# Performance work log

Hardware: AMD Instinct MI355X
Metric: run time of the kernel (lower is better)

The kernel has to match this reference:

```python
import jax, jax.numpy as jnp
import numpy as np

N_NODES = 50000
N_EDGES = 800000
HEADS = 4
IN_CH = 128
HID_CH = 32   # per-head, conv1
OUT_CH = 32   # per-head, conv2
N_GRAPHS = 64
NEG_SLOPE = 0.2
BN_EPS = 1e-5


def gat_conv(x, src, dst, n_nodes, W, att_src, att_dst, bias):
    """PyG-style GATConv (concat heads). x:[N,Fin], W:[Fin,H*C], att_*:[H,C], bias:[H*C]."""
    H, C = att_src.shape
    h = (x @ W).reshape(n_nodes, H, C)                      # [N,H,C]
    a_src = jnp.einsum('nhc,hc->nh', h, att_src)            # [N,H]
    a_dst = jnp.einsum('nhc,hc->nh', h, att_dst)            # [N,H]
    e = jax.nn.leaky_relu(a_src[src] + a_dst[dst], NEG_SLOPE)  # [E,H]
    # segment softmax over incoming edges of each destination node
    e_max = jax.ops.segment_max(e, dst, num_segments=n_nodes)  # [N,H]
    alpha = jnp.exp(e - e_max[dst])                         # [E,H]
    denom = jax.ops.segment_sum(alpha, dst, num_segments=n_nodes)  # [N,H]
    alpha = alpha / denom[dst]
    msg = alpha[:, :, None] * h[src]                        # [E,H,C]
    out = jax.ops.segment_sum(msg, dst, num_segments=n_nodes)  # [N,H,C]
    return out.reshape(n_nodes, H * C) + bias


def setup_inputs() -> dict:
    key = jax.random.key(0)
    ks = jax.random.split(key, 12)
    d1 = HID_CH * HEADS  # 128
    d2 = OUT_CH * HEADS  # 128
    s_in = 1.0 / np.sqrt(IN_CH)
    s_h = 1.0 / np.sqrt(d1)
    return {
        'x': jax.random.normal(ks[0], (N_NODES, IN_CH), jnp.float32),
        'edge_index': jax.random.randint(ks[1], (2, N_EDGES), 0, N_NODES, jnp.int32),
        'batch': jnp.sort(jax.random.randint(ks[2], (N_NODES,), 0, N_GRAPHS, jnp.int32)),
        'W1': jax.random.normal(ks[3], (IN_CH, d1), jnp.float32) * s_in,
        'att_src1': jax.random.normal(ks[4], (HEADS, HID_CH), jnp.float32) * s_h,
        'att_dst1': jax.random.normal(ks[5], (HEADS, HID_CH), jnp.float32) * s_h,
        'bias1': jnp.zeros((d1,), jnp.float32),
        'gamma1': jnp.ones((d1,), jnp.float32),
        'beta1': jnp.zeros((d1,), jnp.float32),
        'W2': jax.random.normal(ks[6], (d1, d2), jnp.float32) * s_h,
        'att_src2': jax.random.normal(ks[7], (HEADS, OUT_CH), jnp.float32) * s_h,
        'att_dst2': jax.random.normal(ks[8], (HEADS, OUT_CH), jnp.float32) * s_h,
        'bias2': jnp.zeros((d2,), jnp.float32),
    }


def reference(x, edge_index, batch, W1, att_src1, att_dst1, bias1,
              gamma1, beta1, W2, att_src2, att_dst2, bias2):
    n = x.shape[0]
    loops = jnp.arange(n, dtype=edge_index.dtype)
    src = jnp.concatenate([edge_index[0], loops])  # add self-loops (PyG default)
    dst = jnp.concatenate([edge_index[1], loops])

    h = gat_conv(x, src, dst, n, W1, att_src1, att_dst1, bias1)
    # BatchNorm1d (batch statistics, biased variance), then ELU; dropout is inference no-op
    mu = h.mean(axis=0)
    var = h.var(axis=0)
    h = (h - mu) * jax.lax.rsqrt(var + BN_EPS) * gamma1 + beta1
    h = jax.nn.elu(h)

    h2 = gat_conv(h, src, dst, n, W2, att_src2, att_dst2, bias2)  # [N, OUT_CH*HEADS]

    # global mean pool over graphs
    ones = jnp.ones((n,), h2.dtype)
    counts = jax.ops.segment_sum(ones, batch, num_segments=N_GRAPHS)
    pooled = jax.ops.segment_sum(h2, batch, num_segments=N_GRAPHS)
    graph_rep = pooled / jnp.maximum(counts, 1.0)[:, None]
    return (h2, graph_rep)
```

## Files before the change

kernel.cpp:

```cpp
#include <hip/hip_runtime.h>

#define NN 50000
#define NE 800000
#define ET 850000
#define NG 64
#define D  128
#define NB 196
#define CAP 5120
#define CHUNK 8192

typedef unsigned short u16;
typedef unsigned int   u32;
typedef short bf16x8 __attribute__((ext_vector_type(8)));
typedef float f32x4  __attribute__((ext_vector_type(4)));

__device__ __forceinline__ u16 f2b(float f){
  u32 u = __float_as_uint(f);
  u32 r = (u + 0x7fffu + ((u >> 16) & 1u)) >> 16;
  return (u16)r;
}
__device__ __forceinline__ u32 pack2(float a, float b){
  return (u32)f2b(a) | ((u32)f2b(b) << 16);
}
__device__ __forceinline__ float lo16f(u32 u){ return __uint_as_float(u << 16); }
__device__ __forceinline__ float hi16f(u32 u){ return __uint_as_float(u & 0xffff0000u); }

__global__ void k_init(int* gCur, float* bsum, float* bsq, float* pooled){
  int i = blockIdx.x*256 + threadIdx.x;
  if (i < 256) gCur[i] = 0;
  if (i < 128){ bsum[i] = 0.f; bsq[i] = 0.f; }
  if (i < NG*D) pooled[i] = 0.f;
}

__global__ __launch_bounds__(256) void k_bucket(const int* __restrict__ srcE, const int* __restrict__ dstE,
                                                int* __restrict__ gCur, int* __restrict__ temp){
  __shared__ int hist[256], hbase[256], hpos[256], gbase[256];
  __shared__ int sorted[CHUNK];
  int tid = threadIdx.x;
  int e0 = blockIdx.x * CHUNK;
  int e1 = e0 + CHUNK; if (e1 > NE) e1 = NE;
  int cnt = e1 - e0;
  hist[tid] = 0;
  __syncthreads();
  for (int i = e0 + tid; i < e1; i += 256)
    atomicAdd(&hist[(u32)dstE[i] >> 8], 1);
  __syncthreads();
  int v = hist[tid];
  hbase[tid] = v;
  __syncthreads();
  for (int off = 1; off < 256; off <<= 1){
    int t = (tid >= off) ? hbase[tid-off] : 0;
    __syncthreads();
    hbase[tid] += t;
    __syncthreads();
  }
  int excl = hbase[tid] - v;
  __syncthreads();
  hbase[tid] = excl;
  hpos[tid]  = excl;
  __syncthreads();
  for (int i = e0 + tid; i < e1; i += 256){
    int d = dstE[i], sr = srcE[i];
    int idx = atomicAdd(&hpos[(u32)d >> 8], 1);
    sorted[idx] = (d << 16) | sr;
  }
  __syncthreads();
  if (tid < NB && hist[tid] > 0)
    gbase[tid] = atomicAdd(&gCur[tid], hist[tid]);
  __syncthreads();
  for (int i = tid; i < cnt; i += 256){
    int vv = sorted[i];
    int b = (u32)vv >> 24;
    int pos = gbase[b] + (i - hbase[b]);
    if (pos < CAP) temp[b*CAP + pos] = vv;
  }
}

__global__ void k_bstart(const int* __restrict__ gCur, int* __restrict__ bstart, int* __restrict__ offs){
  __shared__ int s[256];
  int tid = threadIdx.x;
  int nodes = (tid < NB) ? ((tid == NB-1) ? (NN - (NB-1)*256) : 256) : 0;
  int v = (tid < NB) ? gCur[tid] + nodes : 0;
  s[tid] = v;
  __syncthreads();
  for (int off = 1; off < 256; off <<= 1){
    int t = (tid >= off) ? s[tid-off] : 0;
    __syncthreads();
    s[tid] += t;
    __syncthreads();
  }
  if (tid < NB) bstart[tid] = s[tid] - v;
  if (tid == 0) offs[NN] = ET;
}

__global__ __launch_bounds__(256) void k_place(const int* __restrict__ temp, const int* __restrict__ gCur,
                                               const int* __restrict__ bstart, int* __restrict__ offs,
                                               int* __restrict__ srcs){
  __shared__ int cnt256[256], pfx[256], pos[256];
  int b = blockIdx.x, tid = threadIdx.x;
  int n0 = b << 8;
  int nNodes = NN - n0; if (nNodes > 256) nNodes = 256;
  int count = gCur[b];
  const int* tb = temp + b*CAP;
  cnt256[tid] = 0;
  __syncthreads();
  for (int i = tid; i < count; i += 256)
    atomicAdd(&cnt256[((u32)tb[i] >> 16) & 255], 1);
  __syncthreads();
  int own = cnt256[tid] + (tid < nNodes ? 1 : 0);
  pfx[tid] = own;
  __syncthreads();
  for (int off = 1; off < 256; off <<= 1){
    int t = (tid >= off) ? pfx[tid-off] : 0;
    __syncthreads();
    pfx[tid] += t;
    __syncthreads();
  }
  int excl = pfx[tid] - own;
  __syncthreads();
  pos[tid] = excl + 1;
  __syncthreads();
  int base = bstart[b];
  if (tid < nNodes){
    offs[n0 + tid] = base + excl;
    srcs[base + excl] = n0 + tid;
  }
  for (int i = tid; i < count; i += 256){
    int vv = tb[i];
    int d = ((u32)vv >> 16) & 255;
    int k = atomicAdd(&pos[d], 1);
    srcs[base + k] = vv & 0xFFFF;
  }
}

template<int FUSE_BN>
__global__ __launch_bounds__(512) void k_gemm(const float* __restrict__ X, const float* __restrict__ W,
                                              u16* __restrict__ Ybf,
                                              const float* __restrict__ att_s, const float* __restrict__ att_d,
                                              float* __restrict__ asrc, float* __restrict__ adst,
                                              const float* __restrict__ bsc, const float* __restrict__ bsh,
                                              int nrows){
  __shared__ u16 Xs[64*132];
  __shared__ u16 WT[128*132];
  int tid = threadIdx.x;
  int row0 = blockIdx.x * 64;
  {
    int r = tid >> 3, k4 = tid & 7;
    int gr = row0 + r;
    #pragma unroll
    for (int t = 0; t < 4; t++){
      int kidx = k4 + t*8;
      float4 v = (gr < nrows) ? ((const float4*)(X + (size_t)gr*D))[kidx]
                              : make_float4(0.f,0.f,0.f,0.f);
      if (FUSE_BN){
        float4 sc = ((const float4*)bsc)[kidx];
        float4 sh = ((const float4*)bsh)[kidx];
        v.x = fmaf(v.x, sc.x, sh.x); v.y = fmaf(v.y, sc.y, sh.y);
        v.z = fmaf(v.z, sc.z, sh.z); v.w = fmaf(v.w, sc.w, sh.w);
        v.x = v.x > 0.f ? v.x : expm1f(v.x);
        v.y = v.y > 0.f ? v.y : expm1f(v.y);
        v.z = v.z > 0.f ? v.z : expm1f(v.z);
        v.w = v.w > 0.f ? v.w : expm1f(v.w);
      }
      *(uint2*)&Xs[r*132 + kidx*4] = make_uint2(pack2(v.x, v.y), pack2(v.z, v.w));
    }
  }
  {
    int c = tid & 127, kp = tid >> 7;
    #pragma unroll
    for (int t = 0; t < 16; t++){
      int kk = kp + t*4;
      float w0 = W[(size_t)(2*kk)*D + c];
      float w1 = W[(size_t)(2*kk+1)*D + c];
      *(u32*)&WT[c*132 + 2*kk] = pack2(w0, w1);
    }
  }
  __syncthreads();
  int w = tid >> 6, l = tid & 63;
  int l15 = l & 15, lq = l >> 4;
  int cw = w*16;
  bf16x8 bfr[4];
  #pragma unroll
  for (int ks = 0; ks < 4; ks++)
    bfr[ks] = *(const bf16x8*)&WT[(cw + l15)*132 + ks*32 + lq*8];
  f32x4 acc[4];
  #pragma unroll
  for (int m = 0; m < 4; m++) acc[m] = (f32x4){0.f,0.f,0.f,0.f};
  #pragma unroll
  for (int m = 0; m < 4; m++){
    #pragma unroll
    for (int ks = 0; ks < 4; ks++){
      bf16x8 af = *(const bf16x8*)&Xs[(m*16 + l15)*132 + ks*32 + lq*8];
      acc[m] = __builtin_amdgcn_mfma_f32_16x16x32_bf16(af, bfr[ks], acc[m], 0, 0, 0);
    }
  }
  __syncthreads();
  float* sDotS = (float*)Xs;
  float* sDotD = sDotS + 512;
  {
    float as_c = att_s[cw + l15];
    float ad_c = att_d[cw + l15];
    #pragma unroll
    for (int m = 0; m < 4; m++){
      #pragma unroll
      for (int i = 0; i < 4; i++){
        float ps = acc[m][i] * as_c;
        float pd = acc[m][i] * ad_c;
        #pragma unroll
        for (int msk = 1; msk <= 8; msk <<= 1){
          ps += __shfl_xor(ps, msk);
          pd += __shfl_xor(pd, msk);
        }
        if (l15 == 0){
          int r = m*16 + lq*4 + i;
          sDotS[w*64 + r] = ps;
          sDotD[w*64 + r] = pd;
        }
      }
    }
  }
  #pragma unroll
  for (int m = 0; m < 4; m++){
    #pragma unroll
    for (int i = 0; i < 4; i++){
      float v = acc[m][i];
      float nb = __shfl_xor(v, 1);
      if (!(l & 1)){
        int gr = row0 + m*16 + lq*4 + i;
        if (gr < nrows)
          *(u32*)&Ybf[(size_t)gr*D + cw + l15] = pack2(v, nb);
      }
    }
  }
  __syncthreads();
  if (tid < 256){
    int r = tid >> 2, h = tid & 3;
    int gr = row0 + r;
    if (gr < nrows){
      asrc[gr*4 + h] = sDotS[(2*h)*64 + r] + sDotS[(2*h+1)*64 + r];
      adst[gr*4 + h] = sDotD[(2*h)*64 + r] + sDotD[(2*h+1)*64 + r];
    }
  }
}

__global__ __launch_bounds__(256) void k_edge(
                       const u16* __restrict__ hb, const float* __restrict__ asrc,
                       const float* __restrict__ adst, const int* __restrict__ offs,
                       const int* __restrict__ srcs, const float* __restrict__ bias,
                       float* __restrict__ out){
  __shared__ uint2 sPk[4][4][16];
  int w = threadIdx.x >> 6;
  int lane = threadIdx.x & 63;
  int n = blockIdx.x*4 + w;
  int off0 = offs[n];
  int deg  = offs[n+1] - off0;
  int hd = lane >> 4, j16 = lane & 15;
  float adh = adst[n*4 + hd];
  int half = lane >> 5, q = lane & 31;
  int hg = q >> 3;
  int qb = q*8;
  float denp = 0.f;
  float acc0=0.f, acc1=0.f, acc2=0.f, acc3=0.f;
  const char* hbase = (const char*)hb;
  const int* sp = srcs + off0;
  for (int base = 0; base < deg; base += 16){
    int lim = deg - base; if (lim > 16) lim = 16;
    int sj; float al;
    if (j16 < lim){
      sj = sp[base + j16];
      float e = asrc[sj*4 + hd] + adh;
      e = e > 0.f ? e : 0.2f*e;
      al = __expf(e);
    } else { sj = 0; al = 0.f; }
    denp += al;
    sPk[w][hd][j16] = make_uint2((u32)sj << 8, __float_as_uint(al));
    if (lim == 16){
      uint2 p0 = sPk[w][hg][half],      p1 = sPk[w][hg][2+half];
      uint2 p2 = sPk[w][hg][4+half],    p3 = sPk[w][hg][6+half];
      uint2 p4 = sPk[w][hg][8+half],    p5 = sPk[w][hg][10+half];
      uint2 p6 = sPk[w][hg][12+half],   p7 = sPk[w][hg][14+half];
      uint2 v0 = *(const uint2*)(hbase + p0.x + qb);
      uint2 v1 = *(const uint2*)(hbase + p1.x + qb);
      uint2 v2 = *(const uint2*)(hbase + p2.x + qb);
      uint2 v3 = *(const uint2*)(hbase + p3.x + qb);
      uint2 v4 = *(const uint2*)(hbase + p4.x + qb);
      uint2 v5 = *(const uint2*)(hbase + p5.x + qb);
      uint2 v6 = *(const uint2*)(hbase + p6.x + qb);
      uint2 v7 = *(const uint2*)(hbase + p7.x + qb);
      float a0 = __uint_as_float(p0.y), a1 = __uint_as_float(p1.y);
      float a2 = __uint_as_float(p2.y), a3 = __uint_as_float(p3.y);
      float a4 = __uint_as_float(p4.y), a5 = __uint_as_float(p5.y);
      float a6 = __uint_as_float(p6.y), a7 = __uint_as_float(p7.y);
      acc0 = fmaf(a0, lo16f(v0.x), acc0); acc1 = fmaf(a0, hi16f(v0.x), acc1);
      acc2 = fmaf(a0, lo16f(v0.y), acc2); acc3 = fmaf(a0, hi16f(v0.y), acc3);
      acc0 = fmaf(a1, lo16f(v1.x), acc0); acc1 = fmaf(a1, hi16f(v1.x), acc1);
      acc2 = fmaf(a1, lo16f(v1.y), acc2); acc3 = fmaf(a1, hi16f(v1.y), acc3);
      acc0 = fmaf(a2, lo16f(v2.x), acc0); acc1 = fmaf(a2, hi16f(v2.x), acc1);
      acc2 = fmaf(a2, lo16f(v2.y), acc2); acc3 = fmaf(a2, hi16f(v2.y), acc3);
      acc0 = fmaf(a3, lo16f(v3.x), acc0); acc1 = fmaf(a3, hi16f(v3.x), acc1);
      acc2 = fmaf(a3, lo16f(v3.y), acc2); acc3 = fmaf(a3, hi16f(v3.y), acc3);
      acc0 = fmaf(a4, lo16f(v4.x), acc0); acc1 = fmaf(a4, hi16f(v4.x), acc1);
      acc2 = fmaf(a4, lo16f(v4.y), acc2); acc3 = fmaf(a4, hi16f(v4.y), acc3);
      acc0 = fmaf(a5, lo16f(v5.x), acc0); acc1 = fmaf(a5, hi16f(v5.x), acc1);
      acc2 = fmaf(a5, lo16f(v5.y), acc2); acc3 = fmaf(a5, hi16f(v5.y), acc3);
      acc0 = fmaf(a6, lo16f(v6.x), acc0); acc1 = fmaf(a6, hi16f(v6.x), acc1);
      acc2 = fmaf(a6, lo16f(v6.y), acc2); acc3 = fmaf(a6, hi16f(v6.y), acc3);
      acc0 = fmaf(a7, lo16f(v7.x), acc0); acc1 = fmaf(a7, hi16f(v7.x), acc1);
      acc2 = fmaf(a7, lo16f(v7.y), acc2); acc3 = fmaf(a7, hi16f(v7.y), acc3);
    } else {
      for (int j = 0; j < lim; j += 8){
        uint2 pA = sPk[w][hg][j+half],   pB = sPk[w][hg][j+2+half];
        uint2 pC = sPk[w][hg][j+4+half], pD = sPk[w][hg][j+6+half];
        uint2 vA = *(const uint2*)(hbase + pA.x + qb);
        uint2 vB = *(const uint2*)(hbase + pB.x + qb);
        uint2 vC = *(const uint2*)(hbase + pC.x + qb);
        uint2 vD = *(const uint2*)(hbase + pD.x + qb);
        float aA = __uint_as_float(pA.y), aB = __uint_as_float(pB.y);
        float aC = __uint_as_float(pC.y), aD = __uint_as_float(pD.y);
        acc0 = fmaf(aA, lo16f(vA.x), acc0); acc1 = fmaf(aA, hi16f(vA.x), acc1);
        acc2 = fmaf(aA, lo16f(vA.y), acc2); acc3 = fmaf(aA, hi16f(vA.y), acc3);
        acc0 = fmaf(aB, lo16f(vB.x), acc0); acc1 = fmaf(aB, hi16f(vB.x), acc1);
        acc2 = fmaf(aB, lo16f(vB.y), acc2); acc3 = fmaf(aB, hi16f(vB.y), acc3);
        acc0 = fmaf(aC, lo16f(vC.x), acc0); acc1 = fmaf(aC, hi16f(vC.x), acc1);
        acc2 = fmaf(aC, lo16f(vC.y), acc2); acc3 = fmaf(aC, hi16f(vC.y), acc3);
        acc0 = fmaf(aD, lo16f(vD.x), acc0); acc1 = fmaf(aD, hi16f(vD.x), acc1);
        acc2 = fmaf(aD, lo16f(vD.y), acc2); acc3 = fmaf(aD, hi16f(vD.y), acc3);
      }
    }
  }
  denp += __shfl_xor(denp, 1);
  denp += __shfl_xor(denp, 2);
  denp += __shfl_xor(denp, 4);
  denp += __shfl_xor(denp, 8);
  acc0 += __shfl_xor(acc0, 32);
  acc1 += __shfl_xor(acc1, 32);
  acc2 += __shfl_xor(acc2, 32);
  acc3 += __shfl_xor(acc3, 32);
  float inv = 1.f / __shfl(denp, hg*16);
  if (half == 0){
    int cb = q*4;
    float4 o;
    o.x = acc0*inv + bias[cb];
    o.y = acc1*inv + bias[cb+1];
    o.z = acc2*inv + bias[cb+2];
    o.w = acc3*inv + bias[cb+3];
    ((float4*)(out + (size_t)n*D))[q] = o;
  }
}

__global__ __launch_bounds__(256) void k_bnstat(const float* __restrict__ B,
                                                float* __restrict__ bsum, float* __restrict__ bsq){
  __shared__ float sS[256], sQ[256];
  int tid = threadIdx.x;
  int c = tid & 127;
  int rr = tid >> 7;
  int r0 = blockIdx.x * 64;
  int r1 = r0 + 64; if (r1 > NN) r1 = NN;
  float s = 0.f, qv = 0.f;
  for (int r = r0 + rr; r < r1; r += 2){
    float v = B[(size_t)r*D + c];
    s += v; qv += v*v;
  }
  sS[tid] = s; sQ[tid] = qv;
  __syncthreads();
  if (tid < 128){
    atomicAdd(&bsum[c], sS[tid] + sS[tid+128]);
    atomicAdd(&bsq[c],  sQ[tid] + sQ[tid+128]);
  }
}

__global__ void k_bnfin(const float* __restrict__ bsum, const float* __restrict__ bsq,
                        const float* __restrict__ gamma, const float* __restrict__ beta,
                        float* __restrict__ scale, float* __restrict__ shift){
  int c = threadIdx.x;
  float mu  = bsum[c] * (1.f/NN);
  float var = bsq[c] * (1.f/NN) - mu*mu;
  float sc  = gamma[c] * rsqrtf(var + 1e-5f);
  scale[c] = sc;
  shift[c] = beta[c] - mu*sc;
}

#define POOL_ROWS 50
__global__ void k_poolA(const float* __restrict__ h2, const int* __restrict__ batch,
                        float* __restrict__ pooled){
  int c = threadIdx.x & 127;
  int half = threadIdx.x >> 7;
  int r0 = blockIdx.x * POOL_ROWS;
  int r1 = r0 + POOL_ROWS; if (r1 > NN) r1 = NN;
  float s = 0.f; int g = -1;
  for (int r = r0 + half; r < r1; r += 2){
    int bg = batch[r];
    if (bg != g){
      if (g >= 0) atomicAdd(&pooled[g*D + c], s);
      g = bg; s = 0.f;
    }
    s += h2[(size_t)r*D + c];
  }
  if (g >= 0) atomicAdd(&pooled[g*D + c], s);
}

__global__ void k_poolB(const float* __restrict__ pooled, const int* __restrict__ batch,
                        float* __restrict__ out){
  int g = blockIdx.x;
  int c = threadIdx.x;
  int lo = 0, hi = NN;
  while (lo < hi){ int mid = (lo+hi) >> 1; if (batch[mid] < g) lo = mid+1; else hi = mid; }
  int a = lo, b = NN;
  while (a < b){ int mid = (a+b) >> 1; if (batch[mid] < g+1) a = mid+1; else b = mid; }
  int cntg = a - lo;
  out[g*D + c] = pooled[g*D + c] / (float)(cntg > 1 ? cntg : 1);
}

extern "C" void kernel_launch(void* const* d_in, const int* in_sizes, int n_in,
                              void* d_out, int out_size, void* d_ws, size_t ws_size,
                              hipStream_t stream){
  (void)in_sizes; (void)n_in; (void)out_size; (void)ws_size;
  const float* x   = (const float*)d_in[0];
  const int* ei    = (const int*)d_in[1];
  const int* batch = (const int*)d_in[2];
  const float* W1  = (const float*)d_in[3];
  const float* as1 = (const float*)d_in[4];
  const float* ad1 = (const float*)d_in[5];
  const float* b1  = (const float*)d_in[6];
  const float* g1  = (const float*)d_in[7];
  const float* be1 = (const float*)d_in[8];
  const float* W2  = (const float*)d_in[9];
  const float* as2 = (const float*)d_in[10];
  const float* ad2 = (const float*)d_in[11];
  const float* b2  = (const float*)d_in[12];
  float* outp = (float*)d_out;

  float* B    = (float*)d_ws;
  float* asr  = B + 6400000;
  float* ads  = asr + 200000;
  float* bsum = ads + 200000;
  float* bsq  = bsum + 128;
  float* bsc  = bsq + 128;
  float* bsh  = bsc + 128;
  float* pooled = bsh + 128;
  int* gCur   = (int*)(pooled + NG*D);
  int* bstart = gCur + 256;
  int* offs   = bstart + 256;
  int* srcs   = offs + (NN+1);
  int* temp   = srcs + ET;
  u16* hb     = (u16*)(temp + NB*CAP);

  const int* srcE = ei;
  const int* dstE = ei + NE;

  k_init<<<32, 256, 0, stream>>>(gCur, bsum, bsq, pooled);
  k_gemm<0><<<782, 512, 0, stream>>>(x, W1, hb, as1, ad1, asr, ads, nullptr, nullptr, NN);
  k_bucket<<<(NE + CHUNK - 1)/CHUNK, 256, 0, stream>>>(srcE, dstE, gCur, temp);
  k_bstart<<<1, 256, 0, stream>>>(gCur, bstart, offs);
  k_place<<<NB, 256, 0, stream>>>(temp, gCur, bstart, offs, srcs);
  k_edge<<<NN/4, 256, 0, stream>>>(hb, asr, ads, offs, srcs, b1, B);
  k_bnstat<<<782, 256, 0, stream>>>(B, bsum, bsq);
  k_bnfin<<<1, 128, 0, stream>>>(bsum, bsq, g1, be1, bsc, bsh);
  k_gemm<1><<<782, 512, 0, stream>>>(B, W2, hb, as2, ad2, asr, ads, bsc, bsh, NN);
  k_edge<<<NN/4, 256, 0, stream>>>(hb, asr, ads, offs, srcs, b2, outp);
  k_poolA<<<(NN + POOL_ROWS - 1)/POOL_ROWS, 256, 0, stream>>>(outp, batch, pooled);
  k_poolB<<<NG, 128, 0, stream>>>(pooled, batch, outp + 6400000);
}
```

Baseline: 232.9 us.

## Double GEMM row tile and prefetch next edge chunk indices in edge kernel

The GEMM kernel now handles 128 rows per block instead of 64, halving the grid and amortising the per-block W transpose/load across more rows, at the cost of more LDS and accumulator registers. The edge kernel software-pipelines the neighbour index and asrc gather for the next 16-edge chunk while the current chunk is processed, hiding the dependent load latency. The shared staging array is padded to 17 to reduce LDS bank conflicts. More registers may lower occupancy.

```diff
diff --git a/kernel.cpp b/kernel.cpp
--- a/kernel.cpp
+++ b/kernel.cpp
@@ -140,30 +140,28 @@
                                               float* __restrict__ asrc, float* __restrict__ adst,
                                               const float* __restrict__ bsc, const float* __restrict__ bsh,
                                               int nrows){
-  __shared__ u16 Xs[64*132];
+  __shared__ u16 Xs[128*132];
   __shared__ u16 WT[128*132];
   int tid = threadIdx.x;
-  int row0 = blockIdx.x * 64;
-  {
-    int r = tid >> 3, k4 = tid & 7;
+  int row0 = blockIdx.x * 128;
+  #pragma unroll
+  for (int t = 0; t < 8; t++){
+    int i = tid + t*512;
+    int r = i >> 5, k4 = i & 31;
     int gr = row0 + r;
-    #pragma unroll
-    for (int t = 0; t < 4; t++){
-      int kidx = k4 + t*8;
-      float4 v = (gr < nrows) ? ((const float4*)(X + (size_t)gr*D))[kidx]
-                              : make_float4(0.f,0.f,0.f,0.f);
-      if (FUSE_BN){
-        float4 sc = ((const float4*)bsc)[kidx];
-        float4 sh = ((const float4*)bsh)[kidx];
-        v.x = fmaf(v.x, sc.x, sh.x); v.y = fmaf(v.y, sc.y, sh.y);
-        v.z = fmaf(v.z, sc.z, sh.z); v.w = fmaf(v.w, sc.w, sh.w);
-        v.x = v.x > 0.f ? v.x : expm1f(v.x);
-        v.y = v.y > 0.f ? v.y : expm1f(v.y);
-        v.z = v.z > 0.f ? v.z : expm1f(v.z);
-        v.w = v.w > 0.f ? v.w : expm1f(v.w);
-      }
-      *(uint2*)&Xs[r*132 + kidx*4] = make_uint2(pack2(v.x, v.y), pack2(v.z, v.w));
-    }
+    float4 v = (gr < nrows) ? ((const float4*)(X + (size_t)gr*D))[k4]
+                            : make_float4(0.f,0.f,0.f,0.f);
+    if (FUSE_BN){
+      float4 sc = ((const float4*)bsc)[k4];
+      float4 sh = ((const float4*)bsh)[k4];
+      v.x = fmaf(v.x, sc.x, sh.x); v.y = fmaf(v.y, sc.y, sh.y);
+      v.z = fmaf(v.z, sc.z, sh.z); v.w = fmaf(v.w, sc.w, sh.w);
+      v.x = v.x > 0.f ? v.x : expm1f(v.x);
+      v.y = v.y > 0.f ? v.y : expm1f(v.y);
+      v.z = v.z > 0.f ? v.z : expm1f(v.z);
+      v.w = v.w > 0.f ? v.w : expm1f(v.w);
+    }
+    *(uint2*)&Xs[r*132 + k4*4] = make_uint2(pack2(v.x, v.y), pack2(v.z, v.w));
   }
   {
     int c = tid & 127, kp = tid >> 7;
@@ -183,11 +181,11 @@
   #pragma unroll
   for (int ks = 0; ks < 4; ks++)
     bfr[ks] = *(const bf16x8*)&WT[(cw + l15)*132 + ks*32 + lq*8];
-  f32x4 acc[4];
+  f32x4 acc[8];
   #pragma unroll
-  for (int m = 0; m < 4; m++) acc[m] = (f32x4){0.f,0.f,0.f,0.f};
+  for (int m = 0; m < 8; m++) acc[m] = (f32x4){0.f,0.f,0.f,0.f};
   #pragma unroll
-  for (int m = 0; m < 4; m++){
+  for (int m = 0; m < 8; m++){
     #pragma unroll
     for (int ks = 0; ks < 4; ks++){
       bf16x8 af = *(const bf16x8*)&Xs[(m*16 + l15)*132 + ks*32 + lq*8];
@@ -196,12 +194,12 @@
   }
   __syncthreads();
   float* sDotS = (float*)Xs;
-  float* sDotD = sDotS + 512;
+  float* sDotD = sDotS + 1024;
   {
     float as_c = att_s[cw + l15];
     float ad_c = att_d[cw + l15];
     #pragma unroll
-    for (int m = 0; m < 4; m++){
+    for (int m = 0; m < 8; m++){
       #pragma unroll
       for (int i = 0; i < 4; i++){
         float ps = acc[m][i] * as_c;
@@ -213,14 +211,14 @@
         }
         if (l15 == 0){
           int r = m*16 + lq*4 + i;
-          sDotS[w*64 + r] = ps;
-          sDotD[w*64 + r] = pd;
+          sDotS[w*128 + r] = ps;
+          sDotD[w*128 + r] = pd;
         }
       }
     }
   }
   #pragma unroll
-  for (int m = 0; m < 4; m++){
+  for (int m = 0; m < 8; m++){
     #pragma unroll
     for (int i = 0; i < 4; i++){
       float v = acc[m][i];
@@ -233,12 +231,12 @@
     }
   }
   __syncthreads();
-  if (tid < 256){
+  {
     int r = tid >> 2, h = tid & 3;
     int gr = row0 + r;
     if (gr < nrows){
-      asrc[gr*4 + h] = sDotS[(2*h)*64 + r] + sDotS[(2*h+1)*64 + r];
-      adst[gr*4 + h] = sDotD[(2*h)*64 + r] + sDotD[(2*h+1)*64 + r];
+      asrc[gr*4 + h] = sDotS[(2*h)*128 + r] + sDotS[(2*h+1)*128 + r];
+      adst[gr*4 + h] = sDotD[(2*h)*128 + r] + sDotD[(2*h+1)*128 + r];
     }
   }
 }
@@ -248,7 +246,7 @@
                        const float* __restrict__ adst, const int* __restrict__ offs,
                        const int* __restrict__ srcs, const float* __restrict__ bias,
                        float* __restrict__ out){
-  __shared__ uint2 sPk[4][4][16];
+  __shared__ uint2 sPk[4][4][17];
   int w = threadIdx.x >> 6;
   int lane = threadIdx.x & 63;
   int n = blockIdx.x*4 + w;
@@ -263,17 +261,26 @@
   float acc0=0.f, acc1=0.f, acc2=0.f, acc3=0.f;
   const char* hbase = (const char*)hb;
   const int* sp = srcs + off0;
+  int sj = (j16 < deg) ? sp[j16] : 0;
+  float av = asrc[sj*4 + hd];
   for (int base = 0; base < deg; base += 16){
     int lim = deg - base; if (lim > 16) lim = 16;
-    int sj; float al;
+    int nbase = base + 16;
+    bool hasn = (nbase < deg);
+    int sjn = 0;
+    if (hasn){
+      int idx = nbase + j16;
+      sjn = (idx < deg) ? sp[idx] : 0;
+    }
+    float al;
     if (j16 < lim){
-      sj = sp[base + j16];
-      float e = asrc[sj*4 + hd] + adh;
+      float e = av + adh;
       e = e > 0.f ? e : 0.2f*e;
       al = __expf(e);
-    } else { sj = 0; al = 0.f; }
+    } else al = 0.f;
     denp += al;
     sPk[w][hd][j16] = make_uint2((u32)sj << 8, __float_as_uint(al));
+    float avn = hasn ? asrc[sjn*4 + hd] : 0.f;
     if (lim == 16){
       uint2 p0 = sPk[w][hg][half],      p1 = sPk[w][hg][2+half];
       uint2 p2 = sPk[w][hg][4+half],    p3 = sPk[w][hg][6+half];
@@ -327,6 +334,7 @@
         acc2 = fmaf(aD, lo16f(vD.y), acc2); acc3 = fmaf(aD, hi16f(vD.y), acc3);
       }
     }
+    sj = sjn; av = avn;
   }
   denp += __shfl_xor(denp, 1);
   denp += __shfl_xor(denp, 2);
@@ -449,14 +457,14 @@
   const int* dstE = ei + NE;
 
   k_init<<<32, 256, 0, stream>>>(gCur, bsum, bsq, pooled);
-  k_gemm<0><<<782, 512, 0, stream>>>(x, W1, hb, as1, ad1, asr, ads, nullptr, nullptr, NN);
+  k_gemm<0><<<391, 512, 0, stream>>>(x, W1, hb, as1, ad1, asr, ads, nullptr, nullptr, NN);
   k_bucket<<<(NE + CHUNK - 1)/CHUNK, 256, 0, stream>>>(srcE, dstE, gCur, temp);
   k_bstart<<<1, 256, 0, stream>>>(gCur, bstart, offs);
   k_place<<<NB, 256, 0, stream>>>(temp, gCur, bstart, offs, srcs);
   k_edge<<<NN/4, 256, 0, stream>>>(hb, asr, ads, offs, srcs, b1, B);
   k_bnstat<<<782, 256, 0, stream>>>(B, bsum, bsq);
   k_bnfin<<<1, 128, 0, stream>>>(bsum, bsq, g1, be1, bsc, bsh);
-  k_gemm<1><<<782, 512, 0, stream>>>(B, W2, hb, as2, ad2, asr, ads, bsc, bsh, NN);
+  k_gemm<1><<<391, 512, 0, stream>>>(B, W2, hb, as2, ad2, asr, ads, bsc, bsh, NN);
   k_edge<<<NN/4, 256, 0, stream>>>(hb, asr, ads, offs, srcs, b2, outp);
   k_poolA<<<(NN + POOL_ROWS - 1)/POOL_ROWS, 256, 0, stream>>>(outp, batch, pooled);
   k_poolB<<<NG, 128, 0, stream>>>(pooled, batch, outp + 6400000);
```

Measured after the change: 233.9 us. Within noise of the previous version (+0.4%).
